# Kernel optimization log

Measured on AMD Instinct MI355X. Metric: run time of the kernel, lower is better.

The kernel has to match this reference:

```python
import jax, jax.numpy as jnp
import numpy as np

N_PAPER, N_AUTHOR, N_SUBJECT = 100000, 50000, 5000
N_INP, N_HID, N_OUT = 256, 128, 16
E_PA, E_AP, E_PS, E_SP = 600000, 600000, 200000, 200000


def _seg_mean(msg, dst, n_dst):
    # segment-sum over destination nodes, normalized by in-degree (mean agg)
    s = jax.ops.segment_sum(msg, dst, num_segments=n_dst)
    deg = jax.ops.segment_sum(jnp.ones((dst.shape[0],), msg.dtype), dst, num_segments=n_dst)
    return s / jnp.maximum(deg, 1.0)[:, None]


def _rel_conv(x_src, w, src, dst, n_dst):
    # transform-then-gather (fewer FLOPs than gather-then-transform)
    m = (x_src @ w)[src]  # [E, n_hid]
    return _seg_mean(m, dst, n_dst)


def setup_inputs() -> dict:
    key = jax.random.key(0)
    ks = jax.random.split(key, 32)
    s = 0.05
    inp = {
        'x_paper': jax.random.normal(ks[0], (N_PAPER, N_INP), jnp.float32),
        'x_author': jax.random.normal(ks[1], (N_AUTHOR, N_INP), jnp.float32),
        'x_subject': jax.random.normal(ks[2], (N_SUBJECT, N_INP), jnp.float32),
        'pa_src': jax.random.randint(ks[3], (E_PA,), 0, N_PAPER),
        'pa_dst': jax.random.randint(ks[4], (E_PA,), 0, N_AUTHOR),
        'ap_src': jax.random.randint(ks[5], (E_AP,), 0, N_AUTHOR),
        'ap_dst': jax.random.randint(ks[6], (E_AP,), 0, N_PAPER),
        'ps_src': jax.random.randint(ks[7], (E_PS,), 0, N_PAPER),
        'ps_dst': jax.random.randint(ks[8], (E_PS,), 0, N_SUBJECT),
        'sp_src': jax.random.randint(ks[9], (E_SP,), 0, N_SUBJECT),
        'sp_dst': jax.random.randint(ks[10], (E_SP,), 0, N_PAPER),
        # HeteroAdaptMLP params (per node type, n_layer=1, gelu)
        'enc_w_paper': jax.random.normal(ks[11], (N_INP, N_HID), jnp.float32) * s,
        'enc_b_paper': jnp.zeros((N_HID,), jnp.float32),
        'enc_w_author': jax.random.normal(ks[12], (N_INP, N_HID), jnp.float32) * s,
        'enc_b_author': jnp.zeros((N_HID,), jnp.float32),
        'enc_w_subject': jax.random.normal(ks[13], (N_INP, N_HID), jnp.float32) * s,
        'enc_b_subject': jnp.zeros((N_HID,), jnp.float32),
        # per-relation GraphConv weights, 2 layers x 4 relations
        'w0_pa': jax.random.normal(ks[14], (N_HID, N_HID), jnp.float32) * s,
        'w0_ap': jax.random.normal(ks[15], (N_HID, N_HID), jnp.float32) * s,
        'w0_ps': jax.random.normal(ks[16], (N_HID, N_HID), jnp.float32) * s,
        'w0_sp': jax.random.normal(ks[17], (N_HID, N_HID), jnp.float32) * s,
        'w1_pa': jax.random.normal(ks[18], (N_HID, N_HID), jnp.float32) * s,
        'w1_ap': jax.random.normal(ks[19], (N_HID, N_HID), jnp.float32) * s,
        'w1_ps': jax.random.normal(ks[20], (N_HID, N_HID), jnp.float32) * s,
        'w1_sp': jax.random.normal(ks[21], (N_HID, N_HID), jnp.float32) * s,
        # output head
        'out_w': jax.random.normal(ks[22], (N_HID, N_OUT), jnp.float32) * s,
        'out_b': jnp.zeros((N_OUT,), jnp.float32),
    }
    return inp


def reference(x_paper, x_author, x_subject,
              pa_src, pa_dst, ap_src, ap_dst, ps_src, ps_dst, sp_src, sp_dst,
              enc_w_paper, enc_b_paper, enc_w_author, enc_b_author,
              enc_w_subject, enc_b_subject,
              w0_pa, w0_ap, w0_ps, w0_sp, w1_pa, w1_ap, w1_ps, w1_sp,
              out_w, out_b):
    # task_specific_encoder: per-node-type 1-layer MLP with gelu
    h_p = jax.nn.gelu(x_paper @ enc_w_paper + enc_b_paper)
    h_a = jax.nn.gelu(x_author @ enc_w_author + enc_b_author)
    h_s = jax.nn.gelu(x_subject @ enc_w_subject + enc_b_subject)

    for (w_pa, w_ap, w_ps, w_sp) in ((w0_pa, w0_ap, w0_ps, w0_sp),
                                     (w1_pa, w1_ap, w1_ps, w1_sp)):
        # per-relation gather -> GraphConv(mean) -> scatter; 'sum' across relations
        new_a = _rel_conv(h_p, w_pa, pa_src, pa_dst, N_AUTHOR)
        new_s = _rel_conv(h_p, w_ps, ps_src, ps_dst, N_SUBJECT)
        new_p = (_rel_conv(h_a, w_ap, ap_src, ap_dst, N_PAPER)
                 + _rel_conv(h_s, w_sp, sp_src, sp_dst, N_PAPER))
        # activation=None, self_loop=False, dropout is identity at inference
        h_p, h_a, h_s = new_p, new_a, new_s

    # out_key = 'paper'
    return h_p @ out_w + out_b
```

## Files before the change

### kernel.cpp

```cpp
#include <hip/hip_runtime.h>
#include <math.h>

constexpr int NP = 100000, NA = 50000, NS = 5000;
constexpr int EPA = 600000, EAP = 600000, EPS = 200000, ESP = 200000;
constexpr int ETOT = EPA + EPS + EAP + ESP;
constexpr int NT   = NA + NS + NP + NP;
constexpr int OFF_PS = EPA, OFF_AP = EPA + EPS, OFF_SP = EPA + EPS + EAP;
constexpr int ROW_PS = NA, ROW_AP = NA + NS, ROW_SP = NA + NS + NP;

constexpr int NB_FOLD = 2;
constexpr int NB_PACK = (256*128)/256;
constexpr int NB_HIST = (ETOT + 1023)/1024;
constexpr int HIST_BASE = NB_FOLD + NB_PACK;
constexpr int NB_ENC  = (NP + 63)/64;
constexpr int NB_FILL = (ETOT + 1023)/1024;

typedef short s16x8 __attribute__((ext_vector_type(8)));
typedef float f32x4 __attribute__((ext_vector_type(4)));
typedef unsigned short u16;

__device__ __forceinline__ float gelu_f(float x) {
  float x3 = x*x*x;
  return 0.5f*x*(1.0f + tanhf(0.7978845608028654f*(x + 0.044715f*x3)));
}
__device__ __forceinline__ u16 f2bf(float f) {
  unsigned u = __float_as_uint(f);
  u += 0x7fffu + ((u >> 16) & 1u);
  return (u16)(u >> 16);
}
__device__ __forceinline__ float bf2f(u16 s) {
  return __uint_as_float((unsigned)s << 16);
}

__global__ __launch_bounds__(256) void prep(
    const float* __restrict__ w0_pa, const float* __restrict__ w1_ap,
    const float* __restrict__ w0_ps, const float* __restrict__ w1_sp,
    const float* __restrict__ out_w, u16* __restrict__ WFb,
    const float* __restrict__ ewp, u16* __restrict__ wpk,
    const int* __restrict__ pa_d, const int* __restrict__ ps_d,
    const int* __restrict__ ap_d, const int* __restrict__ sp_d,
    int* __restrict__ h, u16* __restrict__ rank16)
{
  __shared__ float Wst[64*132];
  __shared__ float OW[128*16];
  __shared__ float U[128*16];
  const int b = blockIdx.x, tid = threadIdx.x;

  if (b >= HIST_BASE) {
    const int hblk = b - HIST_BASE;
    const int e = hblk*1024 + tid*4;
    if (e >= ETOT) return;
    const int* dsts; int off;
    if (e < OFF_PS)      { dsts = pa_d;          off = 0; }
    else if (e < OFF_AP) { dsts = ps_d - OFF_PS; off = ROW_PS; }
    else if (e < OFF_SP) { dsts = ap_d - OFF_AP; off = ROW_AP; }
    else                 { dsts = sp_d - OFF_SP; off = ROW_SP; }
    int4 d4 = *(const int4*)(dsts + e);
    unsigned p0 = (unsigned)atomicAdd(&h[off + d4.x], 1);
    unsigned p1 = (unsigned)atomicAdd(&h[off + d4.y], 1);
    unsigned p2 = (unsigned)atomicAdd(&h[off + d4.z], 1);
    unsigned p3 = (unsigned)atomicAdd(&h[off + d4.w], 1);
    uint2 rr;
    rr.x = (p0 & 0xffffu) | (p1 << 16);
    rr.y = (p2 & 0xffffu) | (p3 << 16);
    *(uint2*)(rank16 + e) = rr;
    return;
  }
  if (b >= NB_FOLD) {
    int o = (b - NB_FOLD)*256 + tid;
    int bb = o & 7;
    int l  = (o >> 3) & 63;
    int cf = (o >> 9) & 7;
    int ks = o >> 12;
    wpk[o] = f2bf(ewp[(ks*32 + (l>>4)*8 + bb)*128 + cf*16 + (l & 15)]);
    return;
  }

  const float* w0 = (b == 0) ? w0_pa : w0_ps;
  const float* w1 = (b == 0) ? w1_ap : w1_sp;
  for (int i = tid; i < 512; i += 256) ((float4*)OW)[i] = ((const float4*)out_w)[i];
  for (int half = 0; half < 2; ++half) {
    __syncthreads();
    for (int i = tid; i < 64*32; i += 256) {
      int row = i >> 5, q = i & 31;
      float4 v = ((const float4*)(w1 + (size_t)(half*64 + row)*128))[q];
      *(float4*)&Wst[row*132 + q*4] = v;
    }
    __syncthreads();
    #pragma unroll
    for (int i = 0; i < 4; ++i) {
      int idx = tid + 256*i;
      int r = idx >> 4, c = idx & 15;
      float acc = 0.f;
      #pragma unroll 8
      for (int k = 0; k < 128; ++k) acc = fmaf(Wst[r*132+k], OW[k*16+c], acc);
      U[(half*64 + r)*16 + c] = acc;
    }
  }
  for (int half = 0; half < 2; ++half) {
    __syncthreads();
    for (int i = tid; i < 64*32; i += 256) {
      int row = i >> 5, q = i & 31;
      float4 v = ((const float4*)(w0 + (size_t)(half*64 + row)*128))[q];
      *(float4*)&Wst[row*132 + q*4] = v;
    }
    __syncthreads();
    #pragma unroll
    for (int i = 0; i < 4; ++i) {
      int idx = tid + 256*i;
      int r = idx >> 4, c = idx & 15;
      float acc = 0.f;
      #pragma unroll 8
      for (int k = 0; k < 128; ++k) acc = fmaf(Wst[r*132+k], U[k*16+c], acc);
      int k = half*64 + r;
      int ks = k >> 5;
      int lane = (((k >> 3) & 3) << 4) | c;
      WFb[(((size_t)ks*2 + b)*64 + lane)*8 + (k & 7)] = f2bf(acc);
    }
  }
}

__global__ __launch_bounds__(256) void scan_partial(const int* __restrict__ in, int n,
                                                    int* __restrict__ part) {
  __shared__ int red[4];
  int base = blockIdx.x*4096;
  int sum = 0;
  for (int i = threadIdx.x; i < 4096; i += 256) {
    int idx = base + i;
    sum += (idx < n) ? in[idx] : 0;
  }
  #pragma unroll
  for (int off = 32; off; off >>= 1) sum += __shfl_down(sum, off, 64);
  if ((threadIdx.x & 63) == 0) red[threadIdx.x >> 6] = sum;
  __syncthreads();
  if (threadIdx.x == 0) part[blockIdx.x] = red[0]+red[1]+red[2]+red[3];
}

__global__ __launch_bounds__(256) void scan_chunk(const int* __restrict__ in, int n,
    const int* __restrict__ part, int* __restrict__ out)
{
  int off0 = 0;
  for (int i = 0; i < (int)blockIdx.x; ++i) off0 += part[i];
  const int base = blockIdx.x*4096 + threadIdx.x*16;
  int loc[16]; int s = 0;
  #pragma unroll
  for (int j = 0; j < 16; ++j) {
    int idx = base + j;
    int v = (idx < n) ? in[idx] : 0;
    loc[j] = s; s += v;
  }
  __shared__ int ts[256];
  ts[threadIdx.x] = s; __syncthreads();
  for (int off = 1; off < 256; off <<= 1) {
    int t = (threadIdx.x >= off) ? ts[threadIdx.x - off] : 0;
    __syncthreads();
    ts[threadIdx.x] += t;
    __syncthreads();
  }
  int excl = off0 + ts[threadIdx.x] - s;
  #pragma unroll
  for (int j = 0; j < 16; ++j) {
    int idx = base + j;
    if (idx < n) out[idx] = excl + loc[j];
    if (idx == n-1) out[n] = excl + loc[j] + in[idx];
  }
}

__global__ __launch_bounds__(256) void enc_fill(
    const float* __restrict__ A, const u16* __restrict__ Wp,
    const float* __restrict__ bias, const u16* __restrict__ WFb,
    float* __restrict__ YZ,
    const int* __restrict__ pa_s, const int* __restrict__ pa_d,
    const int* __restrict__ ps_s, const int* __restrict__ ps_d,
    const int* __restrict__ ap_s, const int* __restrict__ ap_d,
    const int* __restrict__ sp_s, const int* __restrict__ sp_d,
    const int* __restrict__ rp, const u16* __restrict__ rank16,
    int* __restrict__ ci)
{
  __shared__ u16 hl[64][136];
  const int b = blockIdx.x;
  const int tid = threadIdx.x;

  if (!(b & 1)) {
    const int fb = b >> 1;
    const int e = fb*1024 + tid*4;
    if (e >= ETOT) return;
    const int *srcs, *dsts; int off;
    if (e < OFF_PS)      { srcs = pa_s;          dsts = pa_d;          off = 0; }
    else if (e < OFF_AP) { srcs = ps_s - OFF_PS; dsts = ps_d - OFF_PS; off = ROW_PS; }
    else if (e < OFF_SP) { srcs = ap_s - OFF_AP; dsts = ap_d - OFF_AP; off = ROW_AP; }
    else                 { srcs = sp_s - OFF_SP; dsts = sp_d - OFF_SP; off = ROW_SP; }
    int4 s4 = *(const int4*)(srcs + e);
    int4 d4 = *(const int4*)(dsts + e);
    uint2 rr = *(const uint2*)(rank16 + e);
    ci[rp[off + d4.x] + (int)(rr.x & 0xffffu)] = s4.x;
    ci[rp[off + d4.y] + (int)(rr.x >> 16)]     = s4.y;
    ci[rp[off + d4.z] + (int)(rr.y & 0xffffu)] = s4.z;
    ci[rp[off + d4.w] + (int)(rr.y >> 16)]     = s4.w;
    return;
  }

  const int eb = b >> 1;
  const int lane = tid & 63, wv = tid >> 6;
  const int rowbase = eb*64 + wv*16;
  const int m  = lane & 15;
  const int kq = lane >> 4;

  f32x4 acc[8];
  #pragma unroll
  for (int j = 0; j < 8; ++j) acc[j] = (f32x4){0.f,0.f,0.f,0.f};

  const int r0 = rowbase + m;
  const bool v0 = r0 < NP;
  const float* Arow = A + (size_t)r0*256 + kq*8;

  #pragma unroll
  for (int ks = 0; ks < 8; ++ks) {
    s16x8 a0 = {0,0,0,0,0,0,0,0};
    if (v0) {
      float4 f = *(const float4*)(Arow + ks*32);
      float4 g = *(const float4*)(Arow + ks*32 + 4);
      a0[0]=(short)f2bf(f.x); a0[1]=(short)f2bf(f.y); a0[2]=(short)f2bf(f.z); a0[3]=(short)f2bf(f.w);
      a0[4]=(short)f2bf(g.x); a0[5]=(short)f2bf(g.y); a0[6]=(short)f2bf(g.z); a0[7]=(short)f2bf(g.w);
    }
    const s16x8* Wf = (const s16x8*)Wp + (size_t)ks*512 + lane;
    #pragma unroll
    for (int cf = 0; cf < 8; ++cf)
      acc[cf] = __builtin_amdgcn_mfma_f32_16x16x32_bf16(a0, Wf[cf*64], acc[cf], 0, 0, 0);
  }

  const int rlb = wv*16 + kq*4;
  #pragma unroll
  for (int cf = 0; cf < 8; ++cf) {
    const int col = cf*16 + m;
    const float bcol = bias[col];
    #pragma unroll
    for (int r = 0; r < 4; ++r)
      hl[rlb + r][col] = f2bf(gelu_f(acc[cf][r] + bcol));
  }
  __syncthreads();

  const s16x8* WFv = (const s16x8*)WFb;
  f32x4 yacc[2];
  yacc[0] = (f32x4){0.f,0.f,0.f,0.f};
  yacc[1] = (f32x4){0.f,0.f,0.f,0.f};
  #pragma unroll
  for (int ks = 0; ks < 4; ++ks) {
    s16x8 af = *(const s16x8*)&hl[wv*16 + m][ks*32 + kq*8];
    yacc[0] = __builtin_amdgcn_mfma_f32_16x16x32_bf16(af, WFv[(ks*2+0)*64 + lane], yacc[0], 0, 0, 0);
    yacc[1] = __builtin_amdgcn_mfma_f32_16x16x32_bf16(af, WFv[(ks*2+1)*64 + lane], yacc[1], 0, 0, 0);
  }

  #pragma unroll
  for (int r = 0; r < 4; ++r) {
    const int row = rowbase + kq*4 + r;
    if (row < NP) {
      YZ[(size_t)row*32 + m]      = yacc[0][r];
      YZ[(size_t)row*32 + 16 + m] = yacc[1][r];
    }
  }
}

__global__ __launch_bounds__(256) void gather16(const float* __restrict__ yz,
    const int* __restrict__ rp, const int* __restrict__ ci,
    float* __restrict__ m16, int n)
{
  int t = blockIdx.x*256 + threadIdx.x;
  int row = t >> 4, lane = t & 15;
  if (row >= n) return;
  int beg = rp[row], end = rp[row+1];
  int off = (row < NA ? 0 : 16) + lane;
  float a = 0.f, b = 0.f;
  int e = beg;
  for (; e + 1 < end; e += 2) {
    a += yz[(size_t)ci[e]  *32 + off];
    b += yz[(size_t)ci[e+1]*32 + off];
  }
  if (e < end) a += yz[(size_t)ci[e]*32 + off];
  int d = end - beg;
  m16[(size_t)row*16 + lane] = (a + b) / (float)(d > 0 ? d : 1);
}

__global__ __launch_bounds__(256) void gather2_16(
    const float* __restrict__ f1, const int* __restrict__ rp1,
    const float* __restrict__ f2, const int* __restrict__ rp2,
    const int* __restrict__ ci, const float* __restrict__ ob,
    float* __restrict__ O, int n)
{
  int t = blockIdx.x*256 + threadIdx.x;
  int row = t >> 4, lane = t & 15;
  if (row >= n) return;

  float s1 = 0.f, s1b = 0.f;
  {
    int beg = rp1[row], end = rp1[row+1];
    int e = beg;
    for (; e + 1 < end; e += 2) {
      s1  += f1[(size_t)ci[e]  *16 + lane];
      s1b += f1[(size_t)ci[e+1]*16 + lane];
    }
    if (e < end) s1 += f1[(size_t)ci[e]*16 + lane];
    int d = end - beg;
    s1 = (s1 + s1b) / (float)(d > 0 ? d : 1);
  }
  float s2 = 0.f, s2b = 0.f;
  {
    int beg = rp2[row], end = rp2[row+1];
    int e = beg;
    for (; e + 1 < end; e += 2) {
      s2  += f2[(size_t)ci[e]  *16 + lane];
      s2b += f2[(size_t)ci[e+1]*16 + lane];
    }
    if (e < end) s2 += f2[(size_t)ci[e]*16 + lane];
    int d = end - beg;
    s2 = (s2 + s2b) / (float)(d > 0 ? d : 1);
  }
  O[(size_t)row*16 + lane] = s1 + s2 + ob[lane];
}

extern "C" void kernel_launch(void* const* d_in, const int* in_sizes, int n_in,
                              void* d_out, int out_size, void* d_ws, size_t ws_size,
                              hipStream_t stream)
{
  const float* x_p = (const float*)d_in[0];
  const int* pa_src=(const int*)d_in[3]; const int* pa_dst=(const int*)d_in[4];
  const int* ap_src=(const int*)d_in[5]; const int* ap_dst=(const int*)d_in[6];
  const int* ps_src=(const int*)d_in[7]; const int* ps_dst=(const int*)d_in[8];
  const int* sp_src=(const int*)d_in[9]; const int* sp_dst=(const int*)d_in[10];
  const float* ewp=(const float*)d_in[11]; const float* ebp=(const float*)d_in[12];
  const float* w0_pa=(const float*)d_in[17];
  const float* w0_ps=(const float*)d_in[19];
  const float* w1_ap=(const float*)d_in[22];
  const float* w1_sp=(const float*)d_in[24];
  const float* out_w=(const float*)d_in[25]; const float* out_b=(const float*)d_in[26];
  float* out = (float*)d_out;

  char* wp = (char*)d_ws;
  auto alloc = [&](size_t bytes) { char* p = wp; wp += (bytes + 255) & ~(size_t)255; return p; };
  float* yz     = (float*)alloc((size_t)NP*32*4);
  int*   ci     = (int*)alloc((size_t)ETOT*4);
  float* m16    = (float*)alloc((size_t)(NA+NS)*16*4);
  u16*   wpk    = (u16*)alloc((size_t)256*128*2);
  u16*   WFb    = (u16*)alloc((size_t)8*64*8*2);
  int*   h      = (int*)alloc((size_t)NT*4);
  u16*   rank16 = (u16*)alloc((size_t)ETOT*2);
  int*   rpG    = (int*)alloc((size_t)(NT+1)*4);
  int*   part   = (int*)alloc((size_t)64*4);

  hipMemsetAsync(h, 0, (size_t)NT*4, stream);
  prep<<<HIST_BASE+NB_HIST,256,0,stream>>>(
      w0_pa, w1_ap, w0_ps, w1_sp, out_w, WFb, ewp, wpk,
      pa_dst, ps_dst, ap_dst, sp_dst, h, rank16);

  int nch = (NT + 4095)/4096;
  scan_partial<<<nch,256,0,stream>>>(h, NT, part);
  scan_chunk  <<<nch,256,0,stream>>>(h, NT, part, rpG);

  enc_fill<<<NB_ENC + NB_FILL,256,0,stream>>>(
      x_p, wpk, ebp, WFb, yz,
      pa_src, pa_dst, ps_src, ps_dst, ap_src, ap_dst, sp_src, sp_dst,
      rpG, rank16, ci);

  gather16<<<(((size_t)(NA+NS)*16)+255)/256,256,0,stream>>>(yz, rpG, ci, m16, NA+NS);

  gather2_16<<<(((size_t)NP*16)+255)/256,256,0,stream>>>(
      m16, rpG + ROW_AP,
      m16 + (size_t)NA*16, rpG + ROW_SP,
      ci, out_b, out, NP);
}
```

Baseline: 219.5 us.

## Regroup kernels to overlap histogram with encoder and CSR fill with gather

Splits the weight fold/pack out of the histogram kernel and fuses the histogram blocks with the encoder GEMM blocks instead. The CSR column fill is split: the pa/ps part runs alone before the first gather, and the ap/sp part is co-scheduled with the first gather, which only reads pa/ps segments. This overlaps independent atomic and scatter work with compute and bandwidth phases. It adds one extra launch and means the encoder now depends on fold_pack finishing first.

```diff
diff --git a/kernel.cpp b/kernel.cpp
--- a/kernel.cpp
+++ b/kernel.cpp
@@ -8,12 +8,13 @@
 constexpr int OFF_PS = EPA, OFF_AP = EPA + EPS, OFF_SP = EPA + EPS + EAP;
 constexpr int ROW_PS = NA, ROW_AP = NA + NS, ROW_SP = NA + NS + NP;
 
-constexpr int NB_FOLD = 2;
-constexpr int NB_PACK = (256*128)/256;
-constexpr int NB_HIST = (ETOT + 1023)/1024;
-constexpr int HIST_BASE = NB_FOLD + NB_PACK;
-constexpr int NB_ENC  = (NP + 63)/64;
-constexpr int NB_FILL = (ETOT + 1023)/1024;
+constexpr int NB_FOLD  = 2;
+constexpr int NB_PACK  = (256*128)/256;
+constexpr int NB_HIST  = (ETOT + 1023)/1024;
+constexpr int NB_ENC   = (NP + 63)/64;
+constexpr int NB_FILLA = (OFF_AP + 1023)/1024;
+constexpr int NB_FILLB = ((ETOT-OFF_AP)+1023)/1024;
+constexpr int NB_G16   = ((NA+NS)*16 + 255)/256;
 
 typedef short s16x8 __attribute__((ext_vector_type(8)));
 typedef float f32x4 __attribute__((ext_vector_type(4)));
@@ -32,23 +33,85 @@
   return __uint_as_float((unsigned)s << 16);
 }
 
-__global__ __launch_bounds__(256) void prep(
+__global__ __launch_bounds__(256) void fold_pack(
     const float* __restrict__ w0_pa, const float* __restrict__ w1_ap,
     const float* __restrict__ w0_ps, const float* __restrict__ w1_sp,
     const float* __restrict__ out_w, u16* __restrict__ WFb,
-    const float* __restrict__ ewp, u16* __restrict__ wpk,
-    const int* __restrict__ pa_d, const int* __restrict__ ps_d,
-    const int* __restrict__ ap_d, const int* __restrict__ sp_d,
-    int* __restrict__ h, u16* __restrict__ rank16)
+    const float* __restrict__ ewp, u16* __restrict__ wpk)
 {
   __shared__ float Wst[64*132];
   __shared__ float OW[128*16];
   __shared__ float U[128*16];
   const int b = blockIdx.x, tid = threadIdx.x;
 
-  if (b >= HIST_BASE) {
-    const int hblk = b - HIST_BASE;
-    const int e = hblk*1024 + tid*4;
+  if (b >= NB_FOLD) {
+    int o = (b - NB_FOLD)*256 + tid;
+    int bb = o & 7;
+    int l  = (o >> 3) & 63;
+    int cf = (o >> 9) & 7;
+    int ks = o >> 12;
+    wpk[o] = f2bf(ewp[(ks*32 + (l>>4)*8 + bb)*128 + cf*16 + (l & 15)]);
+    return;
+  }
+
+  const float* w0 = (b == 0) ? w0_pa : w0_ps;
+  const float* w1 = (b == 0) ? w1_ap : w1_sp;
+  for (int i = tid; i < 512; i += 256) ((float4*)OW)[i] = ((const float4*)out_w)[i];
+  for (int half = 0; half < 2; ++half) {
+    __syncthreads();
+    for (int i = tid; i < 64*32; i += 256) {
+      int row = i >> 5, q = i & 31;
+      float4 v = ((const float4*)(w1 + (size_t)(half*64 + row)*128))[q];
+      *(float4*)&Wst[row*132 + q*4] = v;
+    }
+    __syncthreads();
+    #pragma unroll
+    for (int i = 0; i < 4; ++i) {
+      int idx = tid + 256*i;
+      int r = idx >> 4, c = idx & 15;
+      float acc = 0.f;
+      #pragma unroll 8
+      for (int k = 0; k < 128; ++k) acc = fmaf(Wst[r*132+k], OW[k*16+c], acc);
+      U[(half*64 + r)*16 + c] = acc;
+    }
+  }
+  for (int half = 0; half < 2; ++half) {
+    __syncthreads();
+    for (int i = tid; i < 64*32; i += 256) {
+      int row = i >> 5, q = i & 31;
+      float4 v = ((const float4*)(w0 + (size_t)(half*64 + row)*128))[q];
+      *(float4*)&Wst[row*132 + q*4] = v;
+    }
+    __syncthreads();
+    #pragma unroll
+    for (int i = 0; i < 4; ++i) {
+      int idx = tid + 256*i;
+      int r = idx >> 4, c = idx & 15;
+      float acc = 0.f;
+      #pragma unroll 8
+      for (int k = 0; k < 128; ++k) acc = fmaf(Wst[r*132+k], U[k*16+c], acc);
+      int k = half*64 + r;
+      int ks = k >> 5;
+      int lane = (((k >> 3) & 3) << 4) | c;
+      WFb[(((size_t)ks*2 + b)*64 + lane)*8 + (k & 7)] = f2bf(acc);
+    }
+  }
+}
+
+__global__ __launch_bounds__(256) void hist_enc(
+    const int* __restrict__ pa_d, const int* __restrict__ ps_d,
+    const int* __restrict__ ap_d, const int* __restrict__ sp_d,
+    int* __restrict__ h, u16* __restrict__ rank16,
+    const float* __restrict__ A, const u16* __restrict__ Wp,
+    const float* __restrict__ bias, const u16* __restrict__ WFb,
+    float* __restrict__ YZ)
+{
+  __shared__ u16 hl[64][136];
+  const int b = blockIdx.x;
+  const int tid = threadIdx.x;
+
+  if (!(b & 1)) {
+    const int e = (b >> 1)*1024 + tid*4;
     if (e >= ETOT) return;
     const int* dsts; int off;
     if (e < OFF_PS)      { dsts = pa_d;          off = 0; }
@@ -66,56 +129,63 @@
     *(uint2*)(rank16 + e) = rr;
     return;
   }
-  if (b >= NB_FOLD) {
-    int o = (b - NB_FOLD)*256 + tid;
-    int bb = o & 7;
-    int l  = (o >> 3) & 63;
-    int cf = (o >> 9) & 7;
-    int ks = o >> 12;
-    wpk[o] = f2bf(ewp[(ks*32 + (l>>4)*8 + bb)*128 + cf*16 + (l & 15)]);
-    return;
-  }
-
-  const float* w0 = (b == 0) ? w0_pa : w0_ps;
-  const float* w1 = (b == 0) ? w1_ap : w1_sp;
-  for (int i = tid; i < 512; i += 256) ((float4*)OW)[i] = ((const float4*)out_w)[i];
-  for (int half = 0; half < 2; ++half) {
-    __syncthreads();
-    for (int i = tid; i < 64*32; i += 256) {
-      int row = i >> 5, q = i & 31;
-      float4 v = ((const float4*)(w1 + (size_t)(half*64 + row)*128))[q];
-      *(float4*)&Wst[row*132 + q*4] = v;
-    }
-    __syncthreads();
+
+  const int eb = b >> 1;
+  const int lane = tid & 63, wv = tid >> 6;
+  const int rowbase = eb*64 + wv*16;
+  const int m  = lane & 15;
+  const int kq = lane >> 4;
+
+  f32x4 acc[8];
+  #pragma unroll
+  for (int j = 0; j < 8; ++j) acc[j] = (f32x4){0.f,0.f,0.f,0.f};
+
+  const int r0 = rowbase + m;
+  const bool v0 = r0 < NP;
+  const float* Arow = A + (size_t)r0*256 + kq*8;
+
+  #pragma unroll
+  for (int ks = 0; ks < 8; ++ks) {
+    s16x8 a0 = {0,0,0,0,0,0,0,0};
+    if (v0) {
+      float4 f = *(const float4*)(Arow + ks*32);
+      float4 g = *(const float4*)(Arow + ks*32 + 4);
+      a0[0]=(short)f2bf(f.x); a0[1]=(short)f2bf(f.y); a0[2]=(short)f2bf(f.z); a0[3]=(short)f2bf(f.w);
+      a0[4]=(short)f2bf(g.x); a0[5]=(short)f2bf(g.y); a0[6]=(short)f2bf(g.z); a0[7]=(short)f2bf(g.w);
+    }
+    const s16x8* Wf = (const s16x8*)Wp + (size_t)ks*512 + lane;
     #pragma unroll
-    for (int i = 0; i < 4; ++i) {
-      int idx = tid + 256*i;
-      int r = idx >> 4, c = idx & 15;
-      float acc = 0.f;
-      #pragma unroll 8
-      for (int k = 0; k < 128; ++k) acc = fmaf(Wst[r*132+k], OW[k*16+c], acc);
-      U[(half*64 + r)*16 + c] = acc;
-    }
-  }
-  for (int half = 0; half < 2; ++half) {
-    __syncthreads();
-    for (int i = tid; i < 64*32; i += 256) {
-      int row = i >> 5, q = i & 31;
-      float4 v = ((const float4*)(w0 + (size_t)(half*64 + row)*128))[q];
-      *(float4*)&Wst[row*132 + q*4] = v;
-    }
-    __syncthreads();
+    for (int cf = 0; cf < 8; ++cf)
+      acc[cf] = __builtin_amdgcn_mfma_f32_16x16x32_bf16(a0, Wf[cf*64], acc[cf], 0, 0, 0);
+  }
+
+  const int rlb = wv*16 + kq*4;
+  #pragma unroll
+  for (int cf = 0; cf < 8; ++cf) {
+    const int col = cf*16 + m;
+    const float bcol = bias[col];
     #pragma unroll
-    for (int i = 0; i < 4; ++i) {
-      int idx = tid + 256*i;
-      int r = idx >> 4, c = idx & 15;
-      float acc = 0.f;
-      #pragma unroll 8
-      for (int k = 0; k < 128; ++k) acc = fmaf(Wst[r*132+k], U[k*16+c], acc);
-      int k = half*64 + r;
-      int ks = k >> 5;
-      int lane = (((k >> 3) & 3) << 4) | c;
-      WFb[(((size_t)ks*2 + b)*64 + lane)*8 + (k & 7)] = f2bf(acc);
+    for (int r = 0; r < 4; ++r)
+      hl[rlb + r][col] = f2bf(gelu_f(acc[cf][r] + bcol));
+  }
+  __syncthreads();
+
+  const s16x8* WFv = (const s16x8*)WFb;
+  f32x4 yacc[2];
+  yacc[0] = (f32x4){0.f,0.f,0.f,0.f};
+  yacc[1] = (f32x4){0.f,0.f,0.f,0.f};
+  #pragma unroll
+  for (int ks = 0; ks < 4; ++ks) {
+    s16x8 af = *(const s16x8*)&hl[wv*16 + m][ks*32 + kq*8];
+    yacc[0] = __builtin_amdgcn_mfma_f32_16x16x32_bf16(af, WFv[(ks*2+0)*64 + lane], yacc[0], 0, 0, 0);
+    yacc[1] = __builtin_amdgcn_mfma_f32_16x16x32_bf16(af, WFv[(ks*2+1)*64 + lane], yacc[1], 0, 0, 0);
+  }
+  #pragma unroll
+  for (int r = 0; r < 4; ++r) {
+    const int row = rowbase + kq*4 + r;
+    if (row < NP) {
+      YZ[(size_t)row*32 + m]      = yacc[0][r];
+      YZ[(size_t)row*32 + 16 + m] = yacc[1][r];
     }
   }
 }
@@ -166,10 +236,7 @@
   }
 }
 
-__global__ __launch_bounds__(256) void enc_fill(
-    const float* __restrict__ A, const u16* __restrict__ Wp,
-    const float* __restrict__ bias, const u16* __restrict__ WFb,
-    float* __restrict__ YZ,
+__device__ __forceinline__ void fill4(int e,
     const int* __restrict__ pa_s, const int* __restrict__ pa_d,
     const int* __restrict__ ps_s, const int* __restrict__ ps_d,
     const int* __restrict__ ap_s, const int* __restrict__ ap_d,
@@ -177,108 +244,64 @@
     const int* __restrict__ rp, const u16* __restrict__ rank16,
     int* __restrict__ ci)
 {
-  __shared__ u16 hl[64][136];
+  const int *srcs, *dsts; int off;
+  if (e < OFF_PS)      { srcs = pa_s;          dsts = pa_d;          off = 0; }
+  else if (e < OFF_AP) { srcs = ps_s - OFF_PS; dsts = ps_d - OFF_PS; off = ROW_PS; }
+  else if (e < OFF_SP) { srcs = ap_s - OFF_AP; dsts = ap_d - OFF_AP; off = ROW_AP; }
+  else                 { srcs = sp_s - OFF_SP; dsts = sp_d - OFF_SP; off = ROW_SP; }
+  int4 s4 = *(const int4*)(srcs + e);
+  int4 d4 = *(const int4*)(dsts + e);
+  uint2 rr = *(const uint2*)(rank16 + e);
+  ci[rp[off + d4.x] + (int)(rr.x & 0xffffu)] = s4.x;
+  ci[rp[off + d4.y] + (int)(rr.x >> 16)]     = s4.y;
+  ci[rp[off + d4.z] + (int)(rr.y & 0xffffu)] = s4.z;
+  ci[rp[off + d4.w] + (int)(rr.y >> 16)]     = s4.w;
+}
+
+__global__ __launch_bounds__(256) void fill_paps(
+    const int* __restrict__ pa_s, const int* __restrict__ pa_d,
+    const int* __restrict__ ps_s, const int* __restrict__ ps_d,
+    const int* __restrict__ ap_s, const int* __restrict__ ap_d,
+    const int* __restrict__ sp_s, const int* __restrict__ sp_d,
+    const int* __restrict__ rp, const u16* __restrict__ rank16,
+    int* __restrict__ ci)
+{
+  int e = blockIdx.x*1024 + threadIdx.x*4;
+  if (e < OFF_AP)
+    fill4(e, pa_s, pa_d, ps_s, ps_d, ap_s, ap_d, sp_s, sp_d, rp, rank16, ci);
+}
+
+__global__ __launch_bounds__(256) void g16_fill(
+    const float* __restrict__ yz,
+    const int* __restrict__ rp, const int* __restrict__ ci,
+    float* __restrict__ m16,
+    const int* __restrict__ pa_s, const int* __restrict__ pa_d,
+    const int* __restrict__ ps_s, const int* __restrict__ ps_d,
+    const int* __restrict__ ap_s, const int* __restrict__ ap_d,
+    const int* __restrict__ sp_s, const int* __restrict__ sp_d,
+    const u16* __restrict__ rank16, int* __restrict__ ci_w)
+{
   const int b = blockIdx.x;
-  const int tid = threadIdx.x;
-
-  if (!(b & 1)) {
-    const int fb = b >> 1;
-    const int e = fb*1024 + tid*4;
-    if (e >= ETOT) return;
-    const int *srcs, *dsts; int off;
-    if (e < OFF_PS)      { srcs = pa_s;          dsts = pa_d;          off = 0; }
-    else if (e < OFF_AP) { srcs = ps_s - OFF_PS; dsts = ps_d - OFF_PS; off = ROW_PS; }
-    else if (e < OFF_SP) { srcs = ap_s - OFF_AP; dsts = ap_d - OFF_AP; off = ROW_AP; }
-    else                 { srcs = sp_s - OFF_SP; dsts = sp_d - OFF_SP; off = ROW_SP; }
-    int4 s4 = *(const int4*)(srcs + e);
-    int4 d4 = *(const int4*)(dsts + e);
-    uint2 rr = *(const uint2*)(rank16 + e);
-    ci[rp[off + d4.x] + (int)(rr.x & 0xffffu)] = s4.x;
-    ci[rp[off + d4.y] + (int)(rr.x >> 16)]     = s4.y;
-    ci[rp[off + d4.z] + (int)(rr.y & 0xffffu)] = s4.z;
-    ci[rp[off + d4.w] + (int)(rr.y >> 16)]     = s4.w;
+  if (b < NB_FILLB) {
+    int e = OFF_AP + b*1024 + threadIdx.x*4;
+    if (e < ETOT)
+      fill4(e, pa_s, pa_d, ps_s, ps_d, ap_s, ap_d, sp_s, sp_d, rp, rank16, ci_w);
     return;
   }
-
-  const int eb = b >> 1;
-  const int lane = tid & 63, wv = tid >> 6;
-  const int rowbase = eb*64 + wv*16;
-  const int m  = lane & 15;
-  const int kq = lane >> 4;
-
-  f32x4 acc[8];
-  #pragma unroll
-  for (int j = 0; j < 8; ++j) acc[j] = (f32x4){0.f,0.f,0.f,0.f};
-
-  const int r0 = rowbase + m;
-  const bool v0 = r0 < NP;
-  const float* Arow = A + (size_t)r0*256 + kq*8;
-
-  #pragma unroll
-  for (int ks = 0; ks < 8; ++ks) {
-    s16x8 a0 = {0,0,0,0,0,0,0,0};
-    if (v0) {
-      float4 f = *(const float4*)(Arow + ks*32);
-      float4 g = *(const float4*)(Arow + ks*32 + 4);
-      a0[0]=(short)f2bf(f.x); a0[1]=(short)f2bf(f.y); a0[2]=(short)f2bf(f.z); a0[3]=(short)f2bf(f.w);
-      a0[4]=(short)f2bf(g.x); a0[5]=(short)f2bf(g.y); a0[6]=(short)f2bf(g.z); a0[7]=(short)f2bf(g.w);
-    }
-    const s16x8* Wf = (const s16x8*)Wp + (size_t)ks*512 + lane;
-    #pragma unroll
-    for (int cf = 0; cf < 8; ++cf)
-      acc[cf] = __builtin_amdgcn_mfma_f32_16x16x32_bf16(a0, Wf[cf*64], acc[cf], 0, 0, 0);
-  }
-
-  const int rlb = wv*16 + kq*4;
-  #pragma unroll
-  for (int cf = 0; cf < 8; ++cf) {
-    const int col = cf*16 + m;
-    const float bcol = bias[col];
-    #pragma unroll
-    for (int r = 0; r < 4; ++r)
-      hl[rlb + r][col] = f2bf(gelu_f(acc[cf][r] + bcol));
-  }
-  __syncthreads();
-
-  const s16x8* WFv = (const s16x8*)WFb;
-  f32x4 yacc[2];
-  yacc[0] = (f32x4){0.f,0.f,0.f,0.f};
-  yacc[1] = (f32x4){0.f,0.f,0.f,0.f};
-  #pragma unroll
-  for (int ks = 0; ks < 4; ++ks) {
-    s16x8 af = *(const s16x8*)&hl[wv*16 + m][ks*32 + kq*8];
-    yacc[0] = __builtin_amdgcn_mfma_f32_16x16x32_bf16(af, WFv[(ks*2+0)*64 + lane], yacc[0], 0, 0, 0);
-    yacc[1] = __builtin_amdgcn_mfma_f32_16x16x32_bf16(af, WFv[(ks*2+1)*64 + lane], yacc[1], 0, 0, 0);
-  }
-
-  #pragma unroll
-  for (int r = 0; r < 4; ++r) {
-    const int row = rowbase + kq*4 + r;
-    if (row < NP) {
-      YZ[(size_t)row*32 + m]      = yacc[0][r];
-      YZ[(size_t)row*32 + 16 + m] = yacc[1][r];
-    }
-  }
-}
-
-__global__ __launch_bounds__(256) void gather16(const float* __restrict__ yz,
-    const int* __restrict__ rp, const int* __restrict__ ci,
-    float* __restrict__ m16, int n)
-{
-  int t = blockIdx.x*256 + threadIdx.x;
+  int t = (b - NB_FILLB)*256 + threadIdx.x;
   int row = t >> 4, lane = t & 15;
-  if (row >= n) return;
+  if (row >= NA + NS) return;
   int beg = rp[row], end = rp[row+1];
   int off = (row < NA ? 0 : 16) + lane;
-  float a = 0.f, b = 0.f;
+  float a = 0.f, bb = 0.f;
   int e = beg;
   for (; e + 1 < end; e += 2) {
-    a += yz[(size_t)ci[e]  *32 + off];
-    b += yz[(size_t)ci[e+1]*32 + off];
+    a  += yz[(size_t)ci[e]  *32 + off];
+    bb += yz[(size_t)ci[e+1]*32 + off];
   }
   if (e < end) a += yz[(size_t)ci[e]*32 + off];
   int d = end - beg;
-  m16[(size_t)row*16 + lane] = (a + b) / (float)(d > 0 ? d : 1);
+  m16[(size_t)row*16 + lane] = (a + bb) / (float)(d > 0 ? d : 1);
 }
 
 __global__ __launch_bounds__(256) void gather2_16(
@@ -348,20 +371,25 @@
   int*   part   = (int*)alloc((size_t)64*4);
 
   hipMemsetAsync(h, 0, (size_t)NT*4, stream);
-  prep<<<HIST_BASE+NB_HIST,256,0,stream>>>(
-      w0_pa, w1_ap, w0_ps, w1_sp, out_w, WFb, ewp, wpk,
-      pa_dst, ps_dst, ap_dst, sp_dst, h, rank16);
+  fold_pack<<<NB_FOLD+NB_PACK,256,0,stream>>>(
+      w0_pa, w1_ap, w0_ps, w1_sp, out_w, WFb, ewp, wpk);
+
+  hist_enc<<<NB_HIST+NB_ENC,256,0,stream>>>(
+      pa_dst, ps_dst, ap_dst, sp_dst, h, rank16,
+      x_p, wpk, ebp, WFb, yz);
 
   int nch = (NT + 4095)/4096;
   scan_partial<<<nch,256,0,stream>>>(h, NT, part);
   scan_chunk  <<<nch,256,0,stream>>>(h, NT, part, rpG);
 
-  enc_fill<<<NB_ENC + NB_FILL,256,0,stream>>>(
-      x_p, wpk, ebp, WFb, yz,
+  fill_paps<<<NB_FILLA,256,0,stream>>>(
       pa_src, pa_dst, ps_src, ps_dst, ap_src, ap_dst, sp_src, sp_dst,
       rpG, rank16, ci);
 
-  gather16<<<(((size_t)(NA+NS)*16)+255)/256,256,0,stream>>>(yz, rpG, ci, m16, NA+NS);
+  g16_fill<<<NB_FILLB+NB_G16,256,0,stream>>>(
+      yz, rpG, ci, m16,
+      pa_src, pa_dst, ps_src, ps_dst, ap_src, ap_dst, sp_src, sp_dst,
+      rank16, ci);
 
   gather2_16<<<(((size_t)NP*16)+255)/256,256,0,stream>>>(
       m16, rpG + ROW_AP,
```

After: 200.4 us. -8.7%, faster.
